# Kernel tuning notes

Measured on AMD Instinct MI355X. Metric: run time of the kernel, lower is better.

The kernel has to match this reference:

```python
import jax, jax.numpy as jnp
import numpy as np

N, B, SD, ED = 2048, 64, 512, 512


def setup_inputs() -> dict:
    key = jax.random.key(0)
    k1, k2, k3 = jax.random.split(key, 3)
    state_tm1 = jax.random.normal(k1, (B, SD), dtype=jnp.float32)
    embeddings = jax.random.normal(k2, (N, B, ED), dtype=jnp.float32)
    W = jax.random.normal(k3, (SD + ED, 1), dtype=jnp.float32) * 0.02
    b = jnp.zeros((1,), dtype=jnp.float32)
    return {"state_tm1": state_tm1, "embeddings": embeddings, "W": W, "b": b}


def reference(state_tm1, embeddings, W, b):
    # fc(concat(state, emb)) == state @ W_s + emb @ W_e + b  (split the weight)
    sd = state_tm1.shape[1]
    W_s, W_e = W[:sd], W[sd:]                      # [SD,1], [ED,1]
    state_score = state_tm1 @ W_s + b              # [B,1]
    logits = jnp.einsum('nbe,eo->nbo', embeddings, W_e) + state_score  # [N,B,1]
    alphas = jax.nn.softmax(logits, axis=0)        # softmax over items (dim 0)
    # weighted sum over items: [B, ED]
    return jnp.einsum('nbo,nbe->be', alphas, embeddings)
```

## Files before the change

### kernel.cpp

```cpp
#include <hip/hip_runtime.h>
#include <math.h>

#define BCOL 64
#define ED 512
#define NROWS 2048
#define PARTS 32
#define RPW (NROWS / PARTS)
#define NIT (RPW / 4)

__global__ __launch_bounds__(256, 2)
void attn_partial(const float* __restrict__ emb,
                  const float* __restrict__ W,
                  float* __restrict__ accbuf,
                  float* __restrict__ lbuf)
{
    const int tid  = threadIdx.x;
    const int lane = tid & 63;
    const int wv   = tid >> 6;
    const int col  = blockIdx.x & (BCOL - 1);
    const int part = (blockIdx.x >> 6) * 4 + wv;
    const int grp  = lane >> 4;
    const int q    = lane & 15;

    float4 w[8];
    const float4* We4 = (const float4*)(W + ED);
    #pragma unroll
    for (int k = 0; k < 8; ++k) w[k] = We4[k * 16 + q];

    const size_t rowStride = (size_t)BCOL * ED;
    const int n0 = part * RPW;
    const float* base = emb + ((size_t)(n0 + grp) * BCOL + col) * ED;

    float4 acc[8];
    #pragma unroll
    for (int k = 0; k < 8; ++k) acc[k] = make_float4(0.f, 0.f, 0.f, 0.f);
    float l = 0.f;

    float4 a[8], b[8];
    {
        const float4* rp = (const float4*)base;
        #pragma unroll
        for (int k = 0; k < 8; ++k) a[k] = rp[k * 16 + q];
    }

    for (int i = 0; i < NIT; ++i) {
        const bool more = (i + 1) < NIT;
        if (more) {
            const float4* rp = (const float4*)(base + (size_t)(i + 1) * 4 * rowStride);
            #pragma unroll
            for (int k = 0; k < 8; ++k) b[k] = rp[k * 16 + q];
        }

        float p = 0.f;
        #pragma unroll
        for (int k = 0; k < 8; ++k)
            p += a[k].x * w[k].x + a[k].y * w[k].y
               + a[k].z * w[k].z + a[k].w * w[k].w;
        #pragma unroll
        for (int off = 8; off > 0; off >>= 1)
            p += __shfl_xor(p, off, 64);

        const float pe = __expf(p);
        l += pe;
        #pragma unroll
        for (int k = 0; k < 8; ++k) {
            acc[k].x += pe * a[k].x;
            acc[k].y += pe * a[k].y;
            acc[k].z += pe * a[k].z;
            acc[k].w += pe * a[k].w;
        }

        if (more) {
            #pragma unroll
            for (int k = 0; k < 8; ++k) a[k] = b[k];
        }
    }

    #pragma unroll
    for (int off = 16; off <= 32; off <<= 1) {
        l += __shfl_xor(l, off, 64);
        #pragma unroll
        for (int k = 0; k < 8; ++k) {
            acc[k].x += __shfl_xor(acc[k].x, off, 64);
            acc[k].y += __shfl_xor(acc[k].y, off, 64);
            acc[k].z += __shfl_xor(acc[k].z, off, 64);
            acc[k].w += __shfl_xor(acc[k].w, off, 64);
        }
    }

    if (grp == 0) {
        float4* outp = (float4*)(accbuf + ((size_t)col * PARTS + part) * ED);
        #pragma unroll
        for (int k = 0; k < 8; ++k) outp[k * 16 + q] = acc[k];
        if (q == 0) lbuf[col * PARTS + part] = l;
    }
}

__global__ void attn_reduce(const float* __restrict__ accbuf,
                            const float* __restrict__ lbuf,
                            float* __restrict__ out)
{
    const int col = blockIdx.x;
    const int tid = threadIdx.x;

    __shared__ float Ls;
    if (tid < 64) {
        float lv = (tid < PARTS) ? lbuf[col * PARTS + tid] : 0.f;
        #pragma unroll
        for (int off = 32; off > 0; off >>= 1)
            lv += __shfl_xor(lv, off, 64);
        if (tid == 0) Ls = lv;
    }
    __syncthreads();
    const float inv = 1.0f / Ls;

    const float2* bp = (const float2*)(accbuf + (size_t)col * PARTS * ED);
    float2 s0 = {0.f, 0.f}, s1 = {0.f, 0.f}, s2 = {0.f, 0.f}, s3 = {0.f, 0.f};
    #pragma unroll 1
    for (int g = 0; g < PARTS; g += 4) {
        float2 v0 = bp[(size_t)(g + 0) * (ED / 2) + tid];
        float2 v1 = bp[(size_t)(g + 1) * (ED / 2) + tid];
        float2 v2 = bp[(size_t)(g + 2) * (ED / 2) + tid];
        float2 v3 = bp[(size_t)(g + 3) * (ED / 2) + tid];
        s0.x += v0.x; s0.y += v0.y;  s1.x += v1.x; s1.y += v1.y;
        s2.x += v2.x; s2.y += v2.y;  s3.x += v3.x; s3.y += v3.y;
    }
    float2 r;
    r.x = ((s0.x + s1.x) + (s2.x + s3.x)) * inv;
    r.y = ((s0.y + s1.y) + (s2.y + s3.y)) * inv;
    ((float2*)(out + (size_t)col * ED))[tid] = r;
}

extern "C" void kernel_launch(void* const* d_in, const int* in_sizes, int n_in,
                              void* d_out, int out_size, void* d_ws, size_t ws_size,
                              hipStream_t stream) {
    const float* emb = (const float*)d_in[1];
    const float* W   = (const float*)d_in[2];
    float* out = (float*)d_out;

    float* accbuf = (float*)d_ws;
    float* lbuf = accbuf + (size_t)BCOL * PARTS * ED;

    attn_partial<<<dim3(BCOL * (PARTS / 4)), dim3(256), 0, stream>>>(
        emb, W, accbuf, lbuf);
    attn_reduce<<<dim3(BCOL), dim3(256), 0, stream>>>(accbuf, lbuf, out);
}
```

Before: 370.5 us.

## Use whole-wave rows, double split count, and split reduce across two blocks

```diff
diff --git a/kernel.cpp b/kernel.cpp
--- a/kernel.cpp
+++ b/kernel.cpp
@@ -4,11 +4,11 @@
 #define BCOL 64
 #define ED 512
 #define NROWS 2048
-#define PARTS 32
+#define PARTS 64
 #define RPW (NROWS / PARTS)
-#define NIT (RPW / 4)
+#define RB 4
 
-__global__ __launch_bounds__(256, 2)
+__global__ __launch_bounds__(256, 4)
 void attn_partial(const float* __restrict__ emb,
                   const float* __restrict__ W,
                   float* __restrict__ accbuf,
@@ -19,93 +19,67 @@
     const int wv   = tid >> 6;
     const int col  = blockIdx.x & (BCOL - 1);
     const int part = (blockIdx.x >> 6) * 4 + wv;
-    const int grp  = lane >> 4;
-    const int q    = lane & 15;
 
-    float4 w[8];
     const float4* We4 = (const float4*)(W + ED);
-    #pragma unroll
-    for (int k = 0; k < 8; ++k) w[k] = We4[k * 16 + q];
+    const float4 w0 = We4[lane];
+    const float4 w1 = We4[lane + 64];
+
+    float4 acc0 = {0.f,0.f,0.f,0.f}, acc1 = {0.f,0.f,0.f,0.f};
+    float l = 0.f;
 
     const size_t rowStride = (size_t)BCOL * ED;
-    const int n0 = part * RPW;
-    const float* base = emb + ((size_t)(n0 + grp) * BCOL + col) * ED;
+    const float* base = emb + ((size_t)(part * RPW) * BCOL + col) * ED;
 
-    float4 acc[8];
-    #pragma unroll
-    for (int k = 0; k < 8; ++k) acc[k] = make_float4(0.f, 0.f, 0.f, 0.f);
-    float l = 0.f;
-
-    float4 a[8], b[8];
-    {
-        const float4* rp = (const float4*)base;
+    #pragma unroll 1
+    for (int i = 0; i < RPW; i += RB) {
+        float4 a[RB][2];
         #pragma unroll
-        for (int k = 0; k < 8; ++k) a[k] = rp[k * 16 + q];
-    }
-
-    for (int i = 0; i < NIT; ++i) {
-        const bool more = (i + 1) < NIT;
-        if (more) {
-            const float4* rp = (const float4*)(base + (size_t)(i + 1) * 4 * rowStride);
+        for (int r = 0; r < RB; ++r) {
+            const float4* rp = (const float4*)(base + (size_t)(i + r) * rowStride);
+            a[r][0] = rp[lane];
+            a[r][1] = rp[lane + 64];
+        }
+        float p[RB];
+        #pragma unroll
+        for (int r = 0; r < RB; ++r)
+            p[r] = a[r][0].x*w0.x + a[r][0].y*w0.y + a[r][0].z*w0.z + a[r][0].w*w0.w
+                 + a[r][1].x*w1.x + a[r][1].y*w1.y + a[r][1].z*w1.z + a[r][1].w*w1.w;
+        #pragma unroll
+        for (int off = 32; off > 0; off >>= 1) {
             #pragma unroll
-            for (int k = 0; k < 8; ++k) b[k] = rp[k * 16 + q];
+            for (int r = 0; r < RB; ++r)
+                p[r] += __shfl_xor(p[r], off, 64);
         }
-
-        float p = 0.f;
+        float pe[RB];
         #pragma unroll
-        for (int k = 0; k < 8; ++k)
-            p += a[k].x * w[k].x + a[k].y * w[k].y
-               + a[k].z * w[k].z + a[k].w * w[k].w;
+        for (int r = 0; r < RB; ++r) pe[r] = __expf(p[r]);
+        l += (pe[0] + pe[1]) + (pe[2] + pe[3]);
         #pragma unroll
-        for (int off = 8; off > 0; off >>= 1)
-            p += __shfl_xor(p, off, 64);
-
-        const float pe = __expf(p);
-        l += pe;
-        #pragma unroll
-        for (int k = 0; k < 8; ++k) {
-            acc[k].x += pe * a[k].x;
-            acc[k].y += pe * a[k].y;
-            acc[k].z += pe * a[k].z;
-            acc[k].w += pe * a[k].w;
-        }
-
-        if (more) {
-            #pragma unroll
-            for (int k = 0; k < 8; ++k) a[k] = b[k];
+        for (int r = 0; r < RB; ++r) {
+            acc0.x += pe[r] * a[r][0].x;  acc0.y += pe[r] * a[r][0].y;
+            acc0.z += pe[r] * a[r][0].z;  acc0.w += pe[r] * a[r][0].w;
+            acc1.x += pe[r] * a[r][1].x;  acc1.y += pe[r] * a[r][1].y;
+            acc1.z += pe[r] * a[r][1].z;  acc1.w += pe[r] * a[r][1].w;
         }
     }
 
-    #pragma unroll
-    for (int off = 16; off <= 32; off <<= 1) {
-        l += __shfl_xor(l, off, 64);
-        #pragma unroll
-        for (int k = 0; k < 8; ++k) {
-            acc[k].x += __shfl_xor(acc[k].x, off, 64);
-            acc[k].y += __shfl_xor(acc[k].y, off, 64);
-            acc[k].z += __shfl_xor(acc[k].z, off, 64);
-            acc[k].w += __shfl_xor(acc[k].w, off, 64);
-        }
-    }
-
-    if (grp == 0) {
-        float4* outp = (float4*)(accbuf + ((size_t)col * PARTS + part) * ED);
-        #pragma unroll
-        for (int k = 0; k < 8; ++k) outp[k * 16 + q] = acc[k];
-        if (q == 0) lbuf[col * PARTS + part] = l;
-    }
+    float4* outp = (float4*)(accbuf + ((size_t)col * PARTS + part) * ED);
+    outp[lane]      = acc0;
+    outp[lane + 64] = acc1;
+    if (lane == 0) lbuf[col * PARTS + part] = l;
 }
 
 __global__ void attn_reduce(const float* __restrict__ accbuf,
                             const float* __restrict__ lbuf,
                             float* __restrict__ out)
 {
-    const int col = blockIdx.x;
-    const int tid = threadIdx.x;
+    const int col  = blockIdx.x >> 1;
+    const int half = blockIdx.x & 1;
+    const int tid  = threadIdx.x;
 
     __shared__ float Ls;
     if (tid < 64) {
-        float lv = (tid < PARTS) ? lbuf[col * PARTS + tid] : 0.f;
+        float lv = lbuf[col * PARTS + tid];
         #pragma unroll
         for (int off = 32; off > 0; off >>= 1)
             lv += __shfl_xor(lv, off, 64);
@@ -114,21 +88,17 @@
     __syncthreads();
     const float inv = 1.0f / Ls;
 
-    const float2* bp = (const float2*)(accbuf + (size_t)col * PARTS * ED);
-    float2 s0 = {0.f, 0.f}, s1 = {0.f, 0.f}, s2 = {0.f, 0.f}, s3 = {0.f, 0.f};
+    const int e = half * 256 + tid;
+    const float* bp = accbuf + (size_t)col * PARTS * ED + e;
+    float s0 = 0.f, s1 = 0.f, s2 = 0.f, s3 = 0.f;
     #pragma unroll 1
     for (int g = 0; g < PARTS; g += 4) {
-        float2 v0 = bp[(size_t)(g + 0) * (ED / 2) + tid];
-        float2 v1 = bp[(size_t)(g + 1) * (ED / 2) + tid];
-        float2 v2 = bp[(size_t)(g + 2) * (ED / 2) + tid];
-        float2 v3 = bp[(size_t)(g + 3) * (ED / 2) + tid];
-        s0.x += v0.x; s0.y += v0.y;  s1.x += v1.x; s1.y += v1.y;
-        s2.x += v2.x; s2.y += v2.y;  s3.x += v3.x; s3.y += v3.y;
+        s0 += bp[(size_t)(g + 0) * ED];
+        s1 += bp[(size_t)(g + 1) * ED];
+        s2 += bp[(size_t)(g + 2) * ED];
+        s3 += bp[(size_t)(g + 3) * ED];
     }
-    float2 r;
-    r.x = ((s0.x + s1.x) + (s2.x + s3.x)) * inv;
-    r.y = ((s0.y + s1.y) + (s2.y + s3.y)) * inv;
-    ((float2*)(out + (size_t)col * ED))[tid] = r;
+    out[(size_t)col * ED + e] = ((s0 + s1) + (s2 + s3)) * inv;
 }
 
 extern "C" void kernel_launch(void* const* d_in, const int* in_sizes, int n_in,
@@ -143,5 +113,5 @@
 
     attn_partial<<<dim3(BCOL * (PARTS / 4)), dim3(256), 0, stream>>>(
         emb, W, accbuf, lbuf);
-    attn_reduce<<<dim3(BCOL), dim3(256), 0, stream>>>(accbuf, lbuf, out);
+    attn_reduce<<<dim3(BCOL * 2), dim3(256), 0, stream>>>(accbuf, lbuf, out);
 }
```

Measured after the change: 372.1 us. About the same (+0.4%).
